# Kernel optimization log

Hardware: AMD Instinct MI355X
Metric: run time of the kernel (lower is better)

## Reference

```python
import jax, jax.numpy as jnp
import numpy as np

# lower-triangular <-> 3x3 symmetric matrix index maps (match torch_lotri2mat/mat2lotri)
LOTRI = np.array([[0, 1, 3], [1, 2, 4], [3, 4, 5]])
ROWS = np.array([0, 1, 1, 2, 2, 2])
COLS = np.array([0, 0, 1, 0, 1, 2])
NUM_NEWTON_ITERS = 6


def det3(A):
    # A: (N,3,3)
    return (A[:, 0, 0] * (A[:, 1, 1] * A[:, 2, 2] - A[:, 1, 2] * A[:, 2, 1])
            - A[:, 0, 1] * (A[:, 1, 0] * A[:, 2, 2] - A[:, 1, 2] * A[:, 2, 0])
            + A[:, 0, 2] * (A[:, 1, 0] * A[:, 2, 1] - A[:, 1, 1] * A[:, 2, 0]))


def inv3(A):
    # closed-form 3x3 inverse via adjugate; A: (N,3,3)
    c00 = A[:, 1, 1] * A[:, 2, 2] - A[:, 1, 2] * A[:, 2, 1]
    c01 = A[:, 0, 2] * A[:, 2, 1] - A[:, 0, 1] * A[:, 2, 2]
    c02 = A[:, 0, 1] * A[:, 1, 2] - A[:, 0, 2] * A[:, 1, 1]
    c10 = A[:, 1, 2] * A[:, 2, 0] - A[:, 1, 0] * A[:, 2, 2]
    c11 = A[:, 0, 0] * A[:, 2, 2] - A[:, 0, 2] * A[:, 2, 0]
    c12 = A[:, 0, 2] * A[:, 1, 0] - A[:, 0, 0] * A[:, 1, 2]
    c20 = A[:, 1, 0] * A[:, 2, 1] - A[:, 1, 1] * A[:, 2, 0]
    c21 = A[:, 0, 1] * A[:, 2, 0] - A[:, 0, 0] * A[:, 2, 1]
    c22 = A[:, 0, 0] * A[:, 1, 1] - A[:, 0, 1] * A[:, 1, 0]
    adj = jnp.stack([jnp.stack([c00, c01, c02], -1),
                     jnp.stack([c10, c11, c12], -1),
                     jnp.stack([c20, c21, c22], -1)], -2)  # (N,3,3)
    det = (A[:, 0, 0] * c00 + A[:, 0, 1] * c10 + A[:, 0, 2] * c20)
    return adj / det[:, None, None]


def trilinear_warp(img, ddf):
    # img: (B,C,H,W,D), ddf: (B,3,H,W,D) in voxel units; border padding (clamped corners)
    B, C, H, W, D = img.shape
    base = jnp.stack(jnp.meshgrid(jnp.arange(H), jnp.arange(W), jnp.arange(D),
                                  indexing='ij'), 0).astype(img.dtype)  # (3,H,W,D)
    coords = base[None] + ddf                                           # (B,3,H,W,D)
    c0 = jnp.floor(coords)
    frac = coords - c0
    c0i = c0.astype(jnp.int32)
    dims = jnp.array([H, W, D], jnp.int32).reshape(1, 3, 1, 1, 1)
    lo = jnp.clip(c0i, 0, dims - 1)
    hi = jnp.clip(c0i + 1, 0, dims - 1)
    imgf = img.reshape(B, C, H * W * D)

    def gather(xi, yi, zi):
        lin = (xi * W + yi) * D + zi                      # (B,H,W,D)
        idx = jnp.broadcast_to(lin.reshape(B, 1, -1), (B, C, H * W * D))
        return jnp.take_along_axis(imgf, idx, axis=2).reshape(B, C, H, W, D)

    fx, fy, fz = frac[:, 0, None], frac[:, 1, None], frac[:, 2, None]  # (B,1,H,W,D)
    x0, y0, z0 = lo[:, 0], lo[:, 1], lo[:, 2]
    x1, y1, z1 = hi[:, 0], hi[:, 1], hi[:, 2]
    out = jnp.zeros_like(img)
    for xi, wx in ((x0, 1.0 - fx), (x1, fx)):
        for yi, wy in ((y0, 1.0 - fy), (y1, fy)):
            for zi, wz in ((z0, 1.0 - fz), (z1, fz)):
                out = out + wx * wy * wz * gather(xi, yi, zi)
    return out


def ddf_jacobian(ddf):
    # Jacobian of the deformation phi(x)=x+ddf(x): J = I + d(ddf_i)/dx_j (central differences)
    rows = []
    for i in range(3):
        g = jnp.gradient(ddf[:, i], axis=(1, 2, 3))  # list of 3 arrays (B,H,W,D)
        rows.append(jnp.stack(g, axis=1))
    J = jnp.stack(rows, axis=1)                      # (B,3,3,H,W,D)
    eye = jnp.eye(3, dtype=ddf.dtype).reshape(1, 3, 3, 1, 1, 1)
    return J + eye


def newton_polar_det(X, n_iters):
    # Newton iteration for polar decomposition with determinant scaling
    U = X
    for _ in range(n_iters):
        zeta = jnp.abs(det3(U)) ** (-1.0 / 3.0)
        zU = zeta[:, None, None] * U
        U = 0.5 * (zU + inv3(jnp.swapaxes(zU, -1, -2)))
    return U


def setup_inputs() -> dict:
    key = jax.random.key(0)
    k1, k2 = jax.random.split(key)
    B, H, W, D = 2, 128, 128, 128
    dti = jax.random.normal(k1, (B, 6, H, W, D), dtype=jnp.float32)
    # smooth, realistic displacement field so J = I + grad(ddf) is well-conditioned
    g = jnp.stack(jnp.meshgrid(jnp.arange(H), jnp.arange(W), jnp.arange(D),
                               indexing='ij'), 0).astype(jnp.float32) / H  # (3,H,W,D)
    two_pi = 2.0 * jnp.pi
    amp = 2.0
    ddf = amp * jnp.stack([jnp.sin(two_pi * (g[0] + 0.5 * g[1])),
                           jnp.cos(two_pi * (g[1] + 0.5 * g[2])),
                           jnp.sin(two_pi * (g[2] + 0.5 * g[0]))], 0)  # (3,H,W,D)
    ddf = jnp.broadcast_to(ddf[None], (B, 3, H, W, D))
    ddf = ddf + 0.02 * jax.random.normal(k2, (B, 3, H, W, D), dtype=jnp.float32)
    return {"dti": dti, "ddf": ddf}


def reference(dti, ddf):
    B, _, H, W, D = dti.shape
    # 1) warp the lower-triangular DTI with trilinear interpolation (border padding)
    warped_lotri = trilinear_warp(dti, ddf)              # (B,6,H,W,D)
    # 2) lotri -> 3x3 symmetric matrices, absorb spatial dims
    Dmat = warped_lotri[:, LOTRI]                        # (B,3,3,H,W,D)
    Dns = Dmat.transpose(0, 3, 4, 5, 1, 2).reshape(-1, 3, 3)
    # 3) Jacobian of DDF, absorb spatial dims
    J = ddf_jacobian(ddf)                                # (B,3,3,H,W,D)
    Jns = J.transpose(0, 3, 4, 5, 1, 2).reshape(-1, 3, 3)
    # 4) rotation from polar decomposition (Newton, det scaling)
    R = newton_polar_det(Jns, NUM_NEWTON_ITERS)          # (N,3,3)
    # 5) finite-strain reorientation: R^T D R per voxel
    out_ns = jnp.einsum('nji,njk,nkl->nil', R, Dns, R)
    # 6) expand spatial dims, mat -> lotri
    out_mat = out_ns.reshape(B, H, W, D, 3, 3).transpose(0, 4, 5, 1, 2, 3)
    return out_mat[:, ROWS, COLS]                        # (B,6,H,W,D)
```

## Files before the change

kernel.cpp:

```cpp
#include <hip/hip_runtime.h>

#define NH 128
#define NW 128
#define ND 128
#define HWD (NH * NW * ND)
#define NWD (NW * ND)
#define NB 2

typedef float f32x2 __attribute__((ext_vector_type(2)));

__global__ __launch_bounds__(256) void warp_dti_kernel(
    const float* __restrict__ dti,
    const float* __restrict__ ddf,
    float* __restrict__ out)
{
    const int blk0  = blockIdx.x;
    const int blk   = ((blk0 & 7) << 11) | (blk0 >> 3);

    const int b     = blk >> 13;
    const int blkin = blk & 8191;
    const int tid   = threadIdx.x;
    const int sp    = (blkin << 8) | tid;
    const int d     = tid & (ND - 1);
    const int w     = ((blkin & 63) << 1) | (tid >> 7);
    const int h     = blkin >> 6;

    const int dbase = b * 3 * HWD;

    const int oh_m = (h > 0)      ? -NWD : 0;
    const int oh_p = (h < NH - 1) ?  NWD : 0;
    const int ow_m = (w > 0)      ? -ND  : 0;
    const int ow_p = (w < NW - 1) ?  ND  : 0;
    const int od_m = (d > 0)      ? -1   : 0;
    const int od_p = (d < ND - 1) ?  1   : 0;

    float uc[3], hm[3], hp[3], wm[3], wp[3], dm[3], dp[3];
#pragma unroll
    for (int c = 0; c < 3; ++c) {
        const float* p = ddf + dbase + c * HWD;
        uc[c] = p[sp];
        hm[c] = p[sp + oh_m];  hp[c] = p[sp + oh_p];
        wm[c] = p[sp + ow_m];  wp[c] = p[sp + ow_p];
        dm[c] = p[sp + od_m];  dp[c] = p[sp + od_p];
    }

    const float sh = (oh_m == 0 || oh_p == 0) ? 1.0f : 0.5f;
    const float sw = (ow_m == 0 || ow_p == 0) ? 1.0f : 0.5f;
    const float sd = (od_m == 0 || od_p == 0) ? 1.0f : 0.5f;

    float U[3][3];
#pragma unroll
    for (int c = 0; c < 3; ++c) {
        U[c][0] = sh * (hp[c] - hm[c]);
        U[c][1] = sw * (wp[c] - wm[c]);
        U[c][2] = sd * (dp[c] - dm[c]);
    }
    U[0][0] += 1.0f; U[1][1] += 1.0f; U[2][2] += 1.0f;

    const float cx = (float)h + uc[0];
    const float cy = (float)w + uc[1];
    const float cz = (float)d + uc[2];
    const float flx = floorf(cx), fly = floorf(cy), flz = floorf(cz);
    const float fx = cx - flx, fy = cy - fly, fz = cz - flz;
    const int x0 = (int)flx, y0 = (int)fly, z0 = (int)flz;
    const int xa = min(max(x0,     0), NH - 1), xb = min(max(x0 + 1, 0), NH - 1);
    const int ya = min(max(y0,     0), NW - 1), yb = min(max(y0 + 1, 0), NW - 1);
    const int pa = min(max(z0, 0), ND - 2);

    unsigned voffs[4];
    voffs[0] = (unsigned)(((xa * NW + ya) * ND) + pa) * 4u;
    voffs[1] = (unsigned)(((xa * NW + yb) * ND) + pa) * 4u;
    voffs[2] = (unsigned)(((xb * NW + ya) * ND) + pa) * 4u;
    voffs[3] = (unsigned)(((xb * NW + yb) * ND) + pa) * 4u;

    const float* bases[6];
#pragma unroll
    for (int ch = 0; ch < 6; ++ch)
        bases[ch] = dti + (size_t)(b * 6 + ch) * HWD;

    __builtin_amdgcn_sched_barrier(0);
    f32x2 g[6][4];
#pragma unroll
    for (int ch = 0; ch < 6; ++ch)
#pragma unroll
        for (int c = 0; c < 4; ++c)
            asm volatile("global_load_dwordx2 %0, %1, %2"
                         : "=v"(g[ch][c])
                         : "v"(voffs[c]), "s"(bases[ch]));

#pragma unroll
    for (int it = 0; it < 4; ++it) {
        float c00 = U[1][1]*U[2][2] - U[1][2]*U[2][1];
        float c01 = U[0][2]*U[2][1] - U[0][1]*U[2][2];
        float c02 = U[0][1]*U[1][2] - U[0][2]*U[1][1];
        float c10 = U[1][2]*U[2][0] - U[1][0]*U[2][2];
        float c11 = U[0][0]*U[2][2] - U[0][2]*U[2][0];
        float c12 = U[0][2]*U[1][0] - U[0][0]*U[1][2];
        float c20 = U[1][0]*U[2][1] - U[1][1]*U[2][0];
        float c21 = U[0][1]*U[2][0] - U[0][0]*U[2][1];
        float c22 = U[0][0]*U[1][1] - U[0][1]*U[1][0];
        float det = U[0][0]*c00 + U[0][1]*c10 + U[0][2]*c20;

        float l    = __log2f(fabsf(det));
        float zeta = __builtin_amdgcn_exp2f(-0.33333333333333333f * l);
        float s    = copysignf(zeta * zeta, det);
        float hz = 0.5f * zeta;
        float hs = 0.5f * s;

        float n00 = hz*U[0][0] + c00*hs;
        float n01 = hz*U[0][1] + c10*hs;
        float n02 = hz*U[0][2] + c20*hs;
        float n10 = hz*U[1][0] + c01*hs;
        float n11 = hz*U[1][1] + c11*hs;
        float n12 = hz*U[1][2] + c21*hs;
        float n20 = hz*U[2][0] + c02*hs;
        float n21 = hz*U[2][1] + c12*hs;
        float n22 = hz*U[2][2] + c22*hs;
        U[0][0]=n00; U[0][1]=n01; U[0][2]=n02;
        U[1][0]=n10; U[1][1]=n11; U[1][2]=n12;
        U[2][0]=n20; U[2][1]=n21; U[2][2]=n22;
    }

    const float wza = 1.0f - fz, wzb = fz;
    const float wv0 = ((z0 <= ND - 2) ? wza : 0.0f) + ((z0 <= -1) ? wzb : 0.0f);
    const float wv1 = ((z0 >= ND - 1) ? wza : 0.0f) + ((z0 >=  0) ? wzb : 0.0f);
    const float wxa = 1.0f - fx, wya = 1.0f - fy;
    float wxy[4];
    wxy[0] = wxa * wya;  wxy[1] = wxa * fy;
    wxy[2] = fx  * wya;  wxy[3] = fx  * fy;
    float wA[4], wB[4];
#pragma unroll
    for (int c = 0; c < 4; ++c) { wA[c] = wxy[c] * wv0; wB[c] = wxy[c] * wv1; }

    asm volatile("s_waitcnt vmcnt(0)" ::: "memory");
    __builtin_amdgcn_sched_barrier(0);

    float acc[6] = {0.f, 0.f, 0.f, 0.f, 0.f, 0.f};
#pragma unroll
    for (int c = 0; c < 4; ++c)
#pragma unroll
        for (int ch = 0; ch < 6; ++ch)
            acc[ch] = fmaf(wA[c], g[ch][c].x, fmaf(wB[c], g[ch][c].y, acc[ch]));

    float Dm[3][3];
    Dm[0][0] = acc[0]; Dm[0][1] = acc[1]; Dm[0][2] = acc[3];
    Dm[1][0] = acc[1]; Dm[1][1] = acc[2]; Dm[1][2] = acc[4];
    Dm[2][0] = acc[3]; Dm[2][1] = acc[4]; Dm[2][2] = acc[5];

    float M[3][3];
#pragma unroll
    for (int i = 0; i < 3; ++i)
#pragma unroll
        for (int k = 0; k < 3; ++k)
            M[i][k] = U[0][i]*Dm[0][k] + U[1][i]*Dm[1][k] + U[2][i]*Dm[2][k];

    float T00 = M[0][0]*U[0][0] + M[0][1]*U[1][0] + M[0][2]*U[2][0];
    float T10 = M[1][0]*U[0][0] + M[1][1]*U[1][0] + M[1][2]*U[2][0];
    float T11 = M[1][0]*U[0][1] + M[1][1]*U[1][1] + M[1][2]*U[2][1];
    float T20 = M[2][0]*U[0][0] + M[2][1]*U[1][0] + M[2][2]*U[2][0];
    float T21 = M[2][0]*U[0][1] + M[2][1]*U[1][1] + M[2][2]*U[2][1];
    float T22 = M[2][0]*U[0][2] + M[2][1]*U[1][2] + M[2][2]*U[2][2];

    const int obase = b * 6 * HWD;
    out[obase + 0 * HWD + sp] = T00;
    out[obase + 1 * HWD + sp] = T10;
    out[obase + 2 * HWD + sp] = T11;
    out[obase + 3 * HWD + sp] = T20;
    out[obase + 4 * HWD + sp] = T21;
    out[obase + 5 * HWD + sp] = T22;
}

extern "C" void kernel_launch(void* const* d_in, const int* in_sizes, int n_in,
                              void* d_out, int out_size, void* d_ws, size_t ws_size,
                              hipStream_t stream) {
    const float* dti = (const float*)d_in[0];
    const float* ddf = (const float*)d_in[1];
    float* o = (float*)d_out;
    const int n = NB * HWD;
    warp_dti_kernel<<<n / 256, 256, 0, stream>>>(dti, ddf, o);
}
```

Measured before the change: 270.2 us.

## Process four consecutive voxels per thread with vectorized DDF loads and stores

Each thread now handles four consecutive d-voxels. Neighbor DDF values are loaded as float4 and the d-direction gradient is computed from values already in registers, which cuts redundant stencil loads. Outputs are written as float4 stores. The per-voxel gather loop overlaps the Newton iterations with the DTI loads, but the voxels run sequentially with a full vmcnt wait each, and the grid shrinks fourfold with higher register pressure.

New measurement: 277.5 us. 1.03x slower.

```diff
diff --git a/kernel.cpp b/kernel.cpp
--- a/kernel.cpp
+++ b/kernel.cpp
@@ -8,86 +8,13 @@
 #define NB 2
 
 typedef float f32x2 __attribute__((ext_vector_type(2)));
-
-__global__ __launch_bounds__(256) void warp_dti_kernel(
-    const float* __restrict__ dti,
-    const float* __restrict__ ddf,
-    float* __restrict__ out)
-{
-    const int blk0  = blockIdx.x;
-    const int blk   = ((blk0 & 7) << 11) | (blk0 >> 3);
-
-    const int b     = blk >> 13;
-    const int blkin = blk & 8191;
-    const int tid   = threadIdx.x;
-    const int sp    = (blkin << 8) | tid;
-    const int d     = tid & (ND - 1);
-    const int w     = ((blkin & 63) << 1) | (tid >> 7);
-    const int h     = blkin >> 6;
-
-    const int dbase = b * 3 * HWD;
-
-    const int oh_m = (h > 0)      ? -NWD : 0;
-    const int oh_p = (h < NH - 1) ?  NWD : 0;
-    const int ow_m = (w > 0)      ? -ND  : 0;
-    const int ow_p = (w < NW - 1) ?  ND  : 0;
-    const int od_m = (d > 0)      ? -1   : 0;
-    const int od_p = (d < ND - 1) ?  1   : 0;
-
-    float uc[3], hm[3], hp[3], wm[3], wp[3], dm[3], dp[3];
-#pragma unroll
-    for (int c = 0; c < 3; ++c) {
-        const float* p = ddf + dbase + c * HWD;
-        uc[c] = p[sp];
-        hm[c] = p[sp + oh_m];  hp[c] = p[sp + oh_p];
-        wm[c] = p[sp + ow_m];  wp[c] = p[sp + ow_p];
-        dm[c] = p[sp + od_m];  dp[c] = p[sp + od_p];
-    }
-
-    const float sh = (oh_m == 0 || oh_p == 0) ? 1.0f : 0.5f;
-    const float sw = (ow_m == 0 || ow_p == 0) ? 1.0f : 0.5f;
-    const float sd = (od_m == 0 || od_p == 0) ? 1.0f : 0.5f;
-
-    float U[3][3];
-#pragma unroll
-    for (int c = 0; c < 3; ++c) {
-        U[c][0] = sh * (hp[c] - hm[c]);
-        U[c][1] = sw * (wp[c] - wm[c]);
-        U[c][2] = sd * (dp[c] - dm[c]);
-    }
-    U[0][0] += 1.0f; U[1][1] += 1.0f; U[2][2] += 1.0f;
-
-    const float cx = (float)h + uc[0];
-    const float cy = (float)w + uc[1];
-    const float cz = (float)d + uc[2];
-    const float flx = floorf(cx), fly = floorf(cy), flz = floorf(cz);
-    const float fx = cx - flx, fy = cy - fly, fz = cz - flz;
-    const int x0 = (int)flx, y0 = (int)fly, z0 = (int)flz;
-    const int xa = min(max(x0,     0), NH - 1), xb = min(max(x0 + 1, 0), NH - 1);
-    const int ya = min(max(y0,     0), NW - 1), yb = min(max(y0 + 1, 0), NW - 1);
-    const int pa = min(max(z0, 0), ND - 2);
-
-    unsigned voffs[4];
-    voffs[0] = (unsigned)(((xa * NW + ya) * ND) + pa) * 4u;
-    voffs[1] = (unsigned)(((xa * NW + yb) * ND) + pa) * 4u;
-    voffs[2] = (unsigned)(((xb * NW + ya) * ND) + pa) * 4u;
-    voffs[3] = (unsigned)(((xb * NW + yb) * ND) + pa) * 4u;
-
-    const float* bases[6];
-#pragma unroll
-    for (int ch = 0; ch < 6; ++ch)
-        bases[ch] = dti + (size_t)(b * 6 + ch) * HWD;
-
-    __builtin_amdgcn_sched_barrier(0);
-    f32x2 g[6][4];
-#pragma unroll
-    for (int ch = 0; ch < 6; ++ch)
-#pragma unroll
-        for (int c = 0; c < 4; ++c)
-            asm volatile("global_load_dwordx2 %0, %1, %2"
-                         : "=v"(g[ch][c])
-                         : "v"(voffs[c]), "s"(bases[ch]));
-
+typedef float f32x4 __attribute__((ext_vector_type(4)));
+
+#define SB() __builtin_amdgcn_sched_barrier(0)
+#define LD2(dst, voff, base) asm volatile("global_load_dwordx2 %0, %1, %2" : "=v"(dst) : "v"(voff), "s"(base))
+#define TOUCH(x) asm volatile("" : "+v"(x))
+
+__device__ __forceinline__ void newton4(float U[3][3]) {
 #pragma unroll
     for (int it = 0; it < 4; ++it) {
         float c00 = U[1][1]*U[2][2] - U[1][2]*U[2][1];
@@ -120,54 +47,147 @@
         U[1][0]=n10; U[1][1]=n11; U[1][2]=n12;
         U[2][0]=n20; U[2][1]=n21; U[2][2]=n22;
     }
-
-    const float wza = 1.0f - fz, wzb = fz;
-    const float wv0 = ((z0 <= ND - 2) ? wza : 0.0f) + ((z0 <= -1) ? wzb : 0.0f);
-    const float wv1 = ((z0 >= ND - 1) ? wza : 0.0f) + ((z0 >=  0) ? wzb : 0.0f);
-    const float wxa = 1.0f - fx, wya = 1.0f - fy;
-    float wxy[4];
-    wxy[0] = wxa * wya;  wxy[1] = wxa * fy;
-    wxy[2] = fx  * wya;  wxy[3] = fx  * fy;
-    float wA[4], wB[4];
-#pragma unroll
-    for (int c = 0; c < 4; ++c) { wA[c] = wxy[c] * wv0; wB[c] = wxy[c] * wv1; }
-
-    asm volatile("s_waitcnt vmcnt(0)" ::: "memory");
-    __builtin_amdgcn_sched_barrier(0);
-
-    float acc[6] = {0.f, 0.f, 0.f, 0.f, 0.f, 0.f};
-#pragma unroll
-    for (int c = 0; c < 4; ++c)
+}
+
+__global__ __launch_bounds__(256) void warp_dti_kernel(
+    const float* __restrict__ dti,
+    const float* __restrict__ ddf,
+    float* __restrict__ out)
+{
+    const int blk0 = blockIdx.x;
+    const int blk  = ((blk0 & 7) << 9) | (blk0 >> 3);
+
+    const int b   = blk >> 11;
+    const int h   = (blk >> 4) & 127;
+    const int wg  = blk & 15;
+    const int tid = threadIdx.x;
+    const int w   = (wg << 3) | (tid >> 5);
+    const int d0  = (tid & 31) << 2;
+    const int sp0 = (h << 14) | (w << 7) | d0;
+
+    const float* dch[3];
+    const float* tch[6];
+#pragma unroll
+    for (int c = 0; c < 3; ++c) dch[c] = ddf + (size_t)(b * 3 + c) * HWD;
+#pragma unroll
+    for (int c = 0; c < 6; ++c) tch[c] = dti + (size_t)(b * 6 + c) * HWD;
+
+    const int ohm = (h > 0)      ? -NWD : 0;
+    const int ohp = (h < NH - 1) ?  NWD : 0;
+    const int owm = (w > 0)      ? -ND  : 0;
+    const int owp = (w < NW - 1) ?  ND  : 0;
+    const float sh = (h > 0 && h < NH - 1) ? 0.5f : 1.0f;
+    const float sw = (w > 0 && w < NW - 1) ? 0.5f : 1.0f;
+
+    f32x4 ce[3], hm4[3], hp4[3], wm4[3], wp4[3];
+    float dmv[3], dpv[3];
+#pragma unroll
+    for (int c = 0; c < 3; ++c) {
+        ce[c]  = *reinterpret_cast<const f32x4*>(dch[c] + sp0);
+        hm4[c] = *reinterpret_cast<const f32x4*>(dch[c] + sp0 + ohm);
+        hp4[c] = *reinterpret_cast<const f32x4*>(dch[c] + sp0 + ohp);
+        wm4[c] = *reinterpret_cast<const f32x4*>(dch[c] + sp0 + owm);
+        wp4[c] = *reinterpret_cast<const f32x4*>(dch[c] + sp0 + owp);
+        dmv[c] = dch[c][sp0 + ((d0 > 0)        ? -1 : 0)];
+        dpv[c] = dch[c][sp0 + ((d0 < ND - 4)   ?  4 : 3)];
+    }
+
+    float U[4][3][3];
+    float cxv[4], cyv[4], czv[4];
+#pragma unroll
+    for (int v = 0; v < 4; ++v) {
+#pragma unroll
+        for (int c = 0; c < 3; ++c) {
+            float gd;
+            if (v == 0)      gd = (d0 > 0)      ? 0.5f*(ce[c].y - dmv[c]) : (ce[c].y - ce[c].x);
+            else if (v == 1) gd = 0.5f*(ce[c].z - ce[c].x);
+            else if (v == 2) gd = 0.5f*(ce[c].w - ce[c].y);
+            else             gd = (d0 < ND - 4) ? 0.5f*(dpv[c] - ce[c].z) : (ce[c].w - ce[c].z);
+            U[v][c][0] = sh * (hp4[c][v] - hm4[c][v]);
+            U[v][c][1] = sw * (wp4[c][v] - wm4[c][v]);
+            U[v][c][2] = gd;
+        }
+        U[v][0][0] += 1.0f; U[v][1][1] += 1.0f; U[v][2][2] += 1.0f;
+        cxv[v] = (float)h        + ce[0][v];
+        cyv[v] = (float)w        + ce[1][v];
+        czv[v] = (float)(d0 + v) + ce[2][v];
+    }
+
+    f32x4 Tq[6];
+
+#pragma unroll
+    for (int v = 0; v < 4; ++v) {
+        const float cx = cxv[v], cy = cyv[v], cz = czv[v];
+        const float flx = floorf(cx), fly = floorf(cy), flz = floorf(cz);
+        const float fx = cx - flx, fy = cy - fly, fz = cz - flz;
+        const int x0 = (int)flx, y0 = (int)fly, z0 = (int)flz;
+        const int xa = min(max(x0,     0), NH - 1), xb = min(max(x0 + 1, 0), NH - 1);
+        const int ya = min(max(y0,     0), NW - 1), yb = min(max(y0 + 1, 0), NW - 1);
+        const int pa = min(max(z0, 0), ND - 2);
+
+        unsigned voffs[4];
+        voffs[0] = (unsigned)(((xa * NW + ya) * ND) + pa) * 4u;
+        voffs[1] = (unsigned)(((xa * NW + yb) * ND) + pa) * 4u;
+        voffs[2] = (unsigned)(((xb * NW + ya) * ND) + pa) * 4u;
+        voffs[3] = (unsigned)(((xb * NW + yb) * ND) + pa) * 4u;
+
+        SB();
+        f32x2 g[6][4];
 #pragma unroll
         for (int ch = 0; ch < 6; ++ch)
-            acc[ch] = fmaf(wA[c], g[ch][c].x, fmaf(wB[c], g[ch][c].y, acc[ch]));
-
-    float Dm[3][3];
-    Dm[0][0] = acc[0]; Dm[0][1] = acc[1]; Dm[0][2] = acc[3];
-    Dm[1][0] = acc[1]; Dm[1][1] = acc[2]; Dm[1][2] = acc[4];
-    Dm[2][0] = acc[3]; Dm[2][1] = acc[4]; Dm[2][2] = acc[5];
-
-    float M[3][3];
-#pragma unroll
-    for (int i = 0; i < 3; ++i)
-#pragma unroll
-        for (int k = 0; k < 3; ++k)
-            M[i][k] = U[0][i]*Dm[0][k] + U[1][i]*Dm[1][k] + U[2][i]*Dm[2][k];
-
-    float T00 = M[0][0]*U[0][0] + M[0][1]*U[1][0] + M[0][2]*U[2][0];
-    float T10 = M[1][0]*U[0][0] + M[1][1]*U[1][0] + M[1][2]*U[2][0];
-    float T11 = M[1][0]*U[0][1] + M[1][1]*U[1][1] + M[1][2]*U[2][1];
-    float T20 = M[2][0]*U[0][0] + M[2][1]*U[1][0] + M[2][2]*U[2][0];
-    float T21 = M[2][0]*U[0][1] + M[2][1]*U[1][1] + M[2][2]*U[2][1];
-    float T22 = M[2][0]*U[0][2] + M[2][1]*U[1][2] + M[2][2]*U[2][2];
-
-    const int obase = b * 6 * HWD;
-    out[obase + 0 * HWD + sp] = T00;
-    out[obase + 1 * HWD + sp] = T10;
-    out[obase + 2 * HWD + sp] = T11;
-    out[obase + 3 * HWD + sp] = T20;
-    out[obase + 4 * HWD + sp] = T21;
-    out[obase + 5 * HWD + sp] = T22;
+#pragma unroll
+            for (int c = 0; c < 4; ++c)
+                LD2(g[ch][c], voffs[c], tch[ch]);
+        SB();
+
+        newton4(U[v]);
+
+        const float wza = 1.0f - fz, wzb = fz;
+        const float wv0 = ((z0 <= ND - 2) ? wza : 0.0f) + ((z0 <= -1) ? wzb : 0.0f);
+        const float wv1 = ((z0 >= ND - 1) ? wza : 0.0f) + ((z0 >=  0) ? wzb : 0.0f);
+        const float wxa = 1.0f - fx, wya = 1.0f - fy;
+        float wxy[4];
+        wxy[0] = wxa * wya;  wxy[1] = wxa * fy;
+        wxy[2] = fx  * wya;  wxy[3] = fx  * fy;
+        float wA[4], wB[4];
+#pragma unroll
+        for (int c = 0; c < 4; ++c) { wA[c] = wxy[c] * wv0; wB[c] = wxy[c] * wv1; }
+
+        asm volatile("s_waitcnt vmcnt(0)" ::: "memory");
+        SB();
+#pragma unroll
+        for (int ch = 0; ch < 6; ++ch)
+#pragma unroll
+            for (int c = 0; c < 4; ++c) TOUCH(g[ch][c]);
+
+        float acc[6] = {0.f, 0.f, 0.f, 0.f, 0.f, 0.f};
+#pragma unroll
+        for (int c = 0; c < 4; ++c)
+#pragma unroll
+            for (int ch = 0; ch < 6; ++ch)
+                acc[ch] = fmaf(wA[c], g[ch][c].x, fmaf(wB[c], g[ch][c].y, acc[ch]));
+
+        float Dm00 = acc[0], Dm01 = acc[1], Dm02 = acc[3];
+        float Dm11 = acc[2], Dm12 = acc[4], Dm22 = acc[5];
+        float M[3][3];
+#pragma unroll
+        for (int i = 0; i < 3; ++i) {
+            M[i][0] = U[v][0][i]*Dm00 + U[v][1][i]*Dm01 + U[v][2][i]*Dm02;
+            M[i][1] = U[v][0][i]*Dm01 + U[v][1][i]*Dm11 + U[v][2][i]*Dm12;
+            M[i][2] = U[v][0][i]*Dm02 + U[v][1][i]*Dm12 + U[v][2][i]*Dm22;
+        }
+        Tq[0][v] = M[0][0]*U[v][0][0] + M[0][1]*U[v][1][0] + M[0][2]*U[v][2][0];
+        Tq[1][v] = M[1][0]*U[v][0][0] + M[1][1]*U[v][1][0] + M[1][2]*U[v][2][0];
+        Tq[2][v] = M[1][0]*U[v][0][1] + M[1][1]*U[v][1][1] + M[1][2]*U[v][2][1];
+        Tq[3][v] = M[2][0]*U[v][0][0] + M[2][1]*U[v][1][0] + M[2][2]*U[v][2][0];
+        Tq[4][v] = M[2][0]*U[v][0][1] + M[2][1]*U[v][1][1] + M[2][2]*U[v][2][1];
+        Tq[5][v] = M[2][0]*U[v][0][2] + M[2][1]*U[v][1][2] + M[2][2]*U[v][2][2];
+    }
+
+    float* obase = out + (size_t)b * 6 * HWD + sp0;
+#pragma unroll
+    for (int ch = 0; ch < 6; ++ch)
+        *reinterpret_cast<f32x4*>(obase + (size_t)ch * HWD) = Tq[ch];
 }
 
 extern "C" void kernel_launch(void* const* d_in, const int* in_sizes, int n_in,
@@ -176,6 +196,6 @@
     const float* dti = (const float*)d_in[0];
     const float* ddf = (const float*)d_in[1];
     float* o = (float*)d_out;
-    const int n = NB * HWD;
-    warp_dti_kernel<<<n / 256, 256, 0, stream>>>(dti, ddf, o);
+    const int nblocks = NB * HWD / (256 * 4);
+    warp_dti_kernel<<<nblocks, 256, 0, stream>>>(dti, ddf, o);
 }
```
